# Optimization experiments

Measured on AMD Instinct MI355X. Metric: run time of the kernel, lower is better.

The kernel has to match this reference:

```python
import jax, jax.numpy as jnp
import numpy as np

EMBED = 1024
HEADS = 16
HEAD_DIM = EMBED // HEADS
HIDDEN = 4096
EPS = 1e-5


def setup_inputs() -> dict:
    key = jax.random.key(0)
    ks = jax.random.split(key, 16)
    s_e = 1.0 / np.sqrt(EMBED)
    s_h = 1.0 / np.sqrt(HIDDEN)
    return {
        "x": jax.random.normal(ks[0], (8, 1024, EMBED), dtype=jnp.float32),
        "ln1_g": jnp.ones((EMBED,), jnp.float32),
        "ln1_b": jnp.zeros((EMBED,), jnp.float32),
        "ln2_g": jnp.ones((EMBED,), jnp.float32),
        "ln2_b": jnp.zeros((EMBED,), jnp.float32),
        "wq": jax.random.uniform(ks[1], (EMBED, EMBED), jnp.float32, -s_e, s_e),
        "bq": jax.random.uniform(ks[2], (EMBED,), jnp.float32, -s_e, s_e),
        "wk": jax.random.uniform(ks[3], (EMBED, EMBED), jnp.float32, -s_e, s_e),
        "bk": jax.random.uniform(ks[4], (EMBED,), jnp.float32, -s_e, s_e),
        "wv": jax.random.uniform(ks[5], (EMBED, EMBED), jnp.float32, -s_e, s_e),
        "bv": jax.random.uniform(ks[6], (EMBED,), jnp.float32, -s_e, s_e),
        "wo": jax.random.uniform(ks[7], (EMBED, EMBED), jnp.float32, -s_e, s_e),
        "bo": jax.random.uniform(ks[8], (EMBED,), jnp.float32, -s_e, s_e),
        "w1": jax.random.uniform(ks[9], (EMBED, HIDDEN), jnp.float32, -s_e, s_e),
        "b1": jax.random.uniform(ks[10], (HIDDEN,), jnp.float32, -s_e, s_e),
        "w2": jax.random.uniform(ks[11], (HIDDEN, EMBED), jnp.float32, -s_h, s_h),
        "b2": jax.random.uniform(ks[12], (EMBED,), jnp.float32, -s_h, s_h),
    }


def _layernorm(x, g, b):
    mu = jnp.mean(x, axis=-1, keepdims=True)
    var = jnp.mean((x - mu) ** 2, axis=-1, keepdims=True)
    return (x - mu) * jax.lax.rsqrt(var + EPS) * g + b


def reference(x, ln1_g, ln1_b, ln2_g, ln2_b, wq, bq, wk, bk, wv, bv, wo, bo, w1, b1, w2, b2):
    B, N, E = x.shape
    scale = HEAD_DIM ** (-0.5)
    # --- attention sublayer (pre-norm) ---
    h = _layernorm(x, ln1_g, ln1_b)
    q = (h @ wq + bq).reshape(B, N, HEADS, HEAD_DIM).transpose(0, 2, 1, 3) * scale
    k = (h @ wk + bk).reshape(B, N, HEADS, HEAD_DIM).transpose(0, 2, 1, 3)
    v = (h @ wv + bv).reshape(B, N, HEADS, HEAD_DIM).transpose(0, 2, 1, 3)
    scores = jnp.einsum("bhqd,bhkd->bhqk", q, k)
    attn = jax.nn.softmax(scores, axis=-1)
    ctx = jnp.einsum("bhqk,bhkd->bhqd", attn, v)
    ctx = ctx.transpose(0, 2, 1, 3).reshape(B, N, E)
    x = x + (ctx @ wo + bo)
    # --- FFN sublayer (pre-norm) ---
    h2 = _layernorm(x, ln2_g, ln2_b)
    ff = jax.nn.relu(h2 @ w1 + b1) @ w2 + b2
    return x + ff
```

## Files before the change

kernel.cpp:

```cpp
#include <hip/hip_runtime.h>
#include <hip/hip_bf16.h>

typedef __attribute__((ext_vector_type(4))) float f32x4;
typedef __attribute__((ext_vector_type(8))) __bf16 bf16x8;
typedef __attribute__((ext_vector_type(4))) __bf16 bf16x4;

static constexpr int E    = 1024;
static constexpr int TOK  = 8192;
static constexpr int HID  = 4096;

#define DEVINL __device__ __forceinline__

DEVINL void gload16(const void* g, void* l) {
  __builtin_amdgcn_global_load_lds((__attribute__((address_space(1))) void*)g,
                                   (__attribute__((address_space(3))) void*)l, 16, 0, 0);
}

__global__ __launch_bounds__(256) void wconv_kernel(const float* __restrict__ W,
                                                    __bf16* __restrict__ Wt,
                                                    int K, int N) {
  __shared__ float tile[32][33];
  const int t  = threadIdx.x;
  const long k0 = (long)blockIdx.y * 32;
  const long n0 = (long)blockIdx.x * 32;
  const int r  = t >> 3;
  const int c4 = (t & 7) * 4;
  float4 v = *(const float4*)&W[(k0 + r) * N + n0 + c4];
  tile[r][c4 + 0] = v.x; tile[r][c4 + 1] = v.y;
  tile[r][c4 + 2] = v.z; tile[r][c4 + 3] = v.w;
  __syncthreads();
  bf16x4 o;
#pragma unroll
  for (int i = 0; i < 4; ++i) o[i] = (__bf16)tile[c4 + i][r];
  *(bf16x4*)&Wt[(n0 + r) * K + k0 + c4] = o;
}

__global__ __launch_bounds__(256) void ln_kernel(const float* __restrict__ X,
                                                 const float* __restrict__ g,
                                                 const float* __restrict__ be,
                                                 __bf16* __restrict__ O) {
  const int t = threadIdx.x;
  const long row = blockIdx.x;
  float4 v = *(const float4*)&X[row * E + t * 4];
  float s  = v.x + v.y + v.z + v.w;
  float ss = v.x * v.x + v.y * v.y + v.z * v.z + v.w * v.w;
#pragma unroll
  for (int off = 32; off; off >>= 1) {
    s  += __shfl_down(s, off);
    ss += __shfl_down(ss, off);
  }
  __shared__ float red[8];
  const int w = t >> 6;
  if ((t & 63) == 0) { red[w] = s; red[4 + w] = ss; }
  __syncthreads();
  s  = red[0] + red[1] + red[2] + red[3];
  ss = red[4] + red[5] + red[6] + red[7];
  const float mean = s * (1.0f / E);
  const float var  = ss * (1.0f / E) - mean * mean;
  const float rstd = rsqrtf(var + 1e-5f);
  float4 gv = *(const float4*)&g[t * 4];
  float4 bv = *(const float4*)&be[t * 4];
  bf16x4 o;
  o[0] = (__bf16)((v.x - mean) * rstd * gv.x + bv.x);
  o[1] = (__bf16)((v.y - mean) * rstd * gv.y + bv.y);
  o[2] = (__bf16)((v.z - mean) * rstd * gv.z + bv.z);
  o[3] = (__bf16)((v.w - mean) * rstd * gv.w + bv.w);
  *(bf16x4*)&O[row * E + t * 4] = o;
}

#define ABAR()  asm volatile("s_barrier" ::: "memory")
#define AVM(n)  asm volatile("s_waitcnt vmcnt(" #n ")" ::: "memory")

template <bool RELU, bool RESID, bool OUTBF, int NB>
__global__ __launch_bounds__(512, 2) void gemm8_kernel(const __bf16* __restrict__ A,
                                                       const __bf16* __restrict__ Bt,
                                                       const float* __restrict__ bias0,
                                                       const float* __restrict__ bias1,
                                                       const float* __restrict__ bias2,
                                                       const float* resid,
                                                       void* Cout,
                                                       int M, int N, int K) {
  extern __shared__ char lds[];
  const int tid  = threadIdx.x;
  const int lane = tid & 63;
  const int l15  = lane & 15;
  const int wid  = tid >> 6;
  const int wr   = wid >> 2;
  const int wc   = wid & 3;

  const int nwg  = gridDim.x * gridDim.y;
  const int flat = blockIdx.x + gridDim.x * blockIdx.y;
  const int swz  = (flat & 7) * (nwg >> 3) + (flat >> 3);
  const int bx   = swz % gridDim.x;
  const int by   = swz / gridDim.x;
  const long brow = (long)by * 256;
  const long bcol = (long)bx * 128;

  const __bf16* Ab = A  + brow * K;
  const __bf16* Bb = Bt + bcol * K;
  const int NT = K >> 6;

  char* bA0 = lds;
  char* bA1 = lds + 49152;
  char* bA2 = lds + 98304;

  auto stageA = [&](int k0, char* base, int seg0, int seg1) {
    {
      const int r = seg0 + (tid >> 3);
      const int p = (tid & 7) ^ (r & 7);
      gload16(Ab + (long)r * K + k0 + p * 8, base + seg0 * 128 + tid * 16);
    }
    {
      const int r = seg1 + (tid >> 3);
      const int p = (tid & 7) ^ (r & 7);
      gload16(Ab + (long)r * K + k0 + p * 8, base + seg1 * 128 + tid * 16);
    }
  };
  auto stageB = [&](int k0, char* base) {
#pragma unroll
    for (int i = 0; i < 2; ++i) {
      const int c = i * 64 + (tid >> 3);
      const int p = (tid & 7) ^ (c & 7);
      gload16(Bb + (long)c * K + k0 + p * 8, base + 32768 + i * 8192 + tid * 16);
    }
  };

  f32x4 acc[8][2];
  const f32x4 z4 = {0.f, 0.f, 0.f, 0.f};
#pragma unroll
  for (int m = 0; m < 8; ++m) { acc[m][0] = z4; acc[m][1] = z4; }

  stageA(0, bA0, 0, 128);
  stageA(0, bA0, 64, 192);
  stageB(0, bA0);
  stageA(64, bA1, 0, 128);
  stageA(64, bA1, 64, 192);
  stageB(64, bA1);
  AVM(6);
  ABAR();

  for (int t = 0; t < NT; ++t) {
    const int k2 = (t + 2 < NT) ? ((t + 2) << 6) : 0;

    bf16x8 af[4][2], bfr[2][2];
#pragma unroll
    for (int m = 0; m < 4; ++m)
#pragma unroll
      for (int kk = 0; kk < 2; ++kk) {
        const int row = wr * 128 + m * 16 + l15;
        const int p   = ((kk << 2) + (lane >> 4)) ^ (row & 7);
        af[m][kk] = *(const bf16x8*)(bA0 + row * 128 + p * 16);
      }
#pragma unroll
    for (int n = 0; n < 2; ++n)
#pragma unroll
      for (int kk = 0; kk < 2; ++kk) {
        const int col = wc * 32 + n * 16 + l15;
        const int p   = ((kk << 2) + (lane >> 4)) ^ (col & 7);
        bfr[n][kk] = *(const bf16x8*)(bA0 + 32768 + col * 128 + p * 16);
      }
    stageA(k2, bA2, 0, 128);
    stageB(k2, bA2);
    ABAR();
    __builtin_amdgcn_s_setprio(1);
#pragma unroll
    for (int m = 0; m < 4; ++m)
#pragma unroll
      for (int n = 0; n < 2; ++n) {
        acc[m][n] = __builtin_amdgcn_mfma_f32_16x16x32_bf16(af[m][0], bfr[n][0], acc[m][n], 0, 0, 0);
        acc[m][n] = __builtin_amdgcn_mfma_f32_16x16x32_bf16(af[m][1], bfr[n][1], acc[m][n], 0, 0, 0);
      }
    __builtin_amdgcn_s_setprio(0);
    ABAR();

#pragma unroll
    for (int m = 0; m < 4; ++m)
#pragma unroll
      for (int kk = 0; kk < 2; ++kk) {
        const int row = wr * 128 + (m + 4) * 16 + l15;
        const int p   = ((kk << 2) + (lane >> 4)) ^ (row & 7);
        af[m][kk] = *(const bf16x8*)(bA0 + row * 128 + p * 16);
      }
    stageA(k2, bA2, 64, 192);
    ABAR();
    __builtin_amdgcn_s_setprio(1);
#pragma unroll
    for (int m = 0; m < 4; ++m)
#pragma unroll
      for (int n = 0; n < 2; ++n) {
        acc[m + 4][n] = __builtin_amdgcn_mfma_f32_16x16x32_bf16(af[m][0], bfr[n][0], acc[m + 4][n], 0, 0, 0);
        acc[m + 4][n] = __builtin_amdgcn_mfma_f32_16x16x32_bf16(af[m][1], bfr[n][1], acc[m + 4][n], 0, 0, 0);
      }
    __builtin_amdgcn_s_setprio(0);
    AVM(6);
    ABAR();

    char* tmp = bA0; bA0 = bA1; bA1 = bA2; bA2 = tmp;
  }
  AVM(0);

#pragma unroll
  for (int m = 0; m < 8; ++m) {
#pragma unroll
    for (int n = 0; n < 2; ++n) {
      const long col = bcol + wc * 32 + n * 16 + l15;
      float bb;
      if (NB == 3) {
        const float* bp = (col < 1024) ? bias0 : ((col < 2048) ? bias1 : bias2);
        bb = bp[col & 1023];
      } else {
        bb = bias0[col];
      }
#pragma unroll
      for (int j = 0; j < 4; ++j) {
        const long row = brow + wr * 128 + m * 16 + (lane >> 4) * 4 + j;
        float val = acc[m][n][j] + bb;
        if (RELU) val = fmaxf(val, 0.f);
        const long idx = row * N + col;
        if (RESID) val += resid[idx];
        if (OUTBF) ((__bf16*)Cout)[idx] = (__bf16)val;
        else       ((float*)Cout)[idx]  = val;
      }
    }
  }
}

__global__ __launch_bounds__(256) void attn_kernel(const __bf16* __restrict__ QKV,
                                                   __bf16* __restrict__ Og) {
  __shared__ __align__(16) __bf16 Qs[64 * 64];
  __shared__ __align__(16) __bf16 Ks[64 * 64];
  __shared__ __align__(16) __bf16 Vt[64 * 64];
  __shared__ __align__(16) __bf16 Ps[4 * 16 * 64];

  const int QSTR = 3072;
  const int t    = threadIdx.x;
  const int lane = t & 63;
  const int w    = t >> 6;
  const int b    = blockIdx.y >> 4;
  const int hh   = blockIdx.y & 15;
  const long row0 = (long)b * 1024 + (long)blockIdx.x * 64;
  const int colQ  = hh * 64;
  const int colK  = colQ + 1024;
  const int colV  = colQ + 2048;

#pragma unroll
  for (int j = 0; j < 2; ++j) {
    const int c = j * 256 + t;
    const int r = c >> 3;
    const int p = (c & 7) ^ (r & 7);
    gload16(QKV + (row0 + r) * QSTR + colQ + p * 8, (char*)Qs + c * 16);
  }

  f32x4 ctx[4];
  float m[4], l[4];
  const f32x4 z4 = {0.f, 0.f, 0.f, 0.f};
#pragma unroll
  for (int i = 0; i < 4; ++i) { ctx[i] = z4; m[i] = -INFINITY; l[i] = 0.f; }

  for (int kb = 0; kb < 16; ++kb) {
    __syncthreads();
    const long krow0 = (long)b * 1024 + kb * 64;
#pragma unroll
    for (int j = 0; j < 2; ++j) {
      const int c = j * 256 + t;
      const int r = c >> 3;
      const int p = (c & 7) ^ (r & 7);
      gload16(QKV + (krow0 + r) * QSTR + colK + p * 8, (char*)Ks + c * 16);
    }
#pragma unroll
    for (int j = 0; j < 2; ++j) {
      const int c = j * 256 + t;
      const int key = c >> 3, dc = c & 7;
      bf16x8 vv = *(const bf16x8*)(QKV + (krow0 + key) * QSTR + colV + dc * 8);
#pragma unroll
      for (int e = 0; e < 8; ++e) {
        const int row = dc * 8 + e;
        const int sw  = (row & 7) ^ ((row >> 3) & 7);
        *(__bf16*)((char*)Vt + ((row * 128 + key * 2) ^ (sw << 4))) = vv[e];
      }
    }
    __syncthreads();

    f32x4 s[4];
#pragma unroll
    for (int nf = 0; nf < 4; ++nf) s[nf] = z4;
#pragma unroll
    for (int kk = 0; kk < 2; ++kk) {
      const int qrow = w * 16 + (lane & 15);
      const int qp   = (kk * 4 + (lane >> 4)) ^ (qrow & 7);
      bf16x8 aq = *(const bf16x8*)((const char*)Qs + qrow * 128 + qp * 16);
#pragma unroll
      for (int nf = 0; nf < 4; ++nf) {
        const int krow = nf * 16 + (lane & 15);
        const int kp   = (kk * 4 + (lane >> 4)) ^ (krow & 7);
        bf16x8 bk = *(const bf16x8*)((const char*)Ks + krow * 128 + kp * 16);
        s[nf] = __builtin_amdgcn_mfma_f32_16x16x32_bf16(aq, bk, s[nf], 0, 0, 0);
      }
    }
#pragma unroll
    for (int nf = 0; nf < 4; ++nf)
#pragma unroll
      for (int j = 0; j < 4; ++j) s[nf][j] *= 0.125f;

#pragma unroll
    for (int j = 0; j < 4; ++j) {
      float mx = fmaxf(fmaxf(s[0][j], s[1][j]), fmaxf(s[2][j], s[3][j]));
#pragma unroll
      for (int off = 1; off < 16; off <<= 1) mx = fmaxf(mx, __shfl_xor(mx, off, 16));
      const float mn   = fmaxf(m[j], mx);
      const float corr = __expf(m[j] - mn);
      float rs = 0.f;
      const int prow = (lane >> 4) * 4 + j;
#pragma unroll
      for (int nf = 0; nf < 4; ++nf) {
        const float p = __expf(s[nf][j] - mn);
        rs += p;
        const int col = nf * 16 + (lane & 15);
        *(__bf16*)((char*)Ps + w * 2048 +
                   ((prow * 128 + col * 2) ^ ((prow & 7) << 4))) = (__bf16)p;
      }
#pragma unroll
      for (int off = 1; off < 16; off <<= 1) rs += __shfl_xor(rs, off, 16);
      l[j] = l[j] * corr + rs;
      m[j] = mn;
#pragma unroll
      for (int df = 0; df < 4; ++df) ctx[df][j] *= corr;
    }

#pragma unroll
    for (int kk = 0; kk < 2; ++kk) {
      const int prow = lane & 15;
      const int pp   = (kk * 4 + (lane >> 4)) ^ (prow & 7);
      bf16x8 ap = *(const bf16x8*)((const char*)Ps + w * 2048 + prow * 128 + pp * 16);
#pragma unroll
      for (int df = 0; df < 4; ++df) {
        const int vrow = df * 16 + (lane & 15);
        const int sw   = (vrow & 7) ^ ((vrow >> 3) & 7);
        const int vp   = (kk * 4 + (lane >> 4)) ^ sw;
        bf16x8 bv = *(const bf16x8*)((const char*)Vt + vrow * 128 + vp * 16);
        ctx[df] = __builtin_amdgcn_mfma_f32_16x16x32_bf16(ap, bv, ctx[df], 0, 0, 0);
      }
    }
  }

#pragma unroll
  for (int df = 0; df < 4; ++df)
#pragma unroll
    for (int j = 0; j < 4; ++j) {
      const long row = row0 + w * 16 + (lane >> 4) * 4 + j;
      const int  col = colQ + df * 16 + (lane & 15);
      Og[row * E + col] = (__bf16)(ctx[df][j] / l[j]);
    }
}

extern "C" void kernel_launch(void* const* d_in, const int* in_sizes, int n_in,
                              void* d_out, int out_size, void* d_ws, size_t ws_size,
                              hipStream_t stream) {
  const float* x     = (const float*)d_in[0];
  const float* ln1g  = (const float*)d_in[1];
  const float* ln1b  = (const float*)d_in[2];
  const float* ln2g  = (const float*)d_in[3];
  const float* ln2b  = (const float*)d_in[4];
  const float* wq    = (const float*)d_in[5];
  const float* bq    = (const float*)d_in[6];
  const float* wk    = (const float*)d_in[7];
  const float* bk    = (const float*)d_in[8];
  const float* wv    = (const float*)d_in[9];
  const float* bv    = (const float*)d_in[10];
  const float* wo    = (const float*)d_in[11];
  const float* bo    = (const float*)d_in[12];
  const float* w1    = (const float*)d_in[13];
  const float* b1    = (const float*)d_in[14];
  const float* w2    = (const float*)d_in[15];
  const float* b2    = (const float*)d_in[16];
  float* out = (float*)d_out;

  char* ws = (char*)d_ws;
  const size_t MB = 1024 * 1024;
  __bf16* Wqkv = (__bf16*)(ws + 0 * MB);
  __bf16* Wot  = (__bf16*)(ws + 6 * MB);
  __bf16* W1t  = (__bf16*)(ws + 8 * MB);
  __bf16* W2t  = (__bf16*)(ws + 16 * MB);
  __bf16* h    = (__bf16*)(ws + 24 * MB);
  __bf16* qkv  = (__bf16*)(ws + 40 * MB);
  __bf16* ctx  = (__bf16*)(ws + 88 * MB);
  __bf16* ff1  = (__bf16*)(ws + 40 * MB);

  const dim3 blk(256);
  const dim3 blk512(512);
  const size_t GLDS = 147456;

  wconv_kernel<<<dim3(E / 32, E / 32), blk, 0, stream>>>(wq, Wqkv, E, E);
  wconv_kernel<<<dim3(E / 32, E / 32), blk, 0, stream>>>(wk, Wqkv + 1024 * 1024, E, E);
  wconv_kernel<<<dim3(E / 32, E / 32), blk, 0, stream>>>(wv, Wqkv + 2048 * 1024, E, E);
  wconv_kernel<<<dim3(E / 32, E / 32), blk, 0, stream>>>(wo, Wot, E, E);
  wconv_kernel<<<dim3(HID / 32, E / 32), blk, 0, stream>>>(w1, W1t, E, HID);
  wconv_kernel<<<dim3(E / 32, HID / 32), blk, 0, stream>>>(w2, W2t, HID, E);

  ln_kernel<<<TOK, blk, 0, stream>>>(x, ln1g, ln1b, h);

  gemm8_kernel<false, false, true, 3><<<dim3(3072 / 128, TOK / 256), blk512, GLDS, stream>>>(
      h, Wqkv, bq, bk, bv, nullptr, qkv, TOK, 3072, E);

  attn_kernel<<<dim3(16, 128), blk, 0, stream>>>(qkv, ctx);

  gemm8_kernel<false, true, false, 1><<<dim3(E / 128, TOK / 256), blk512, GLDS, stream>>>(
      ctx, Wot, bo, nullptr, nullptr, x, out, TOK, E, E);

  ln_kernel<<<TOK, blk, 0, stream>>>(out, ln2g, ln2b, h);

  gemm8_kernel<true, false, true, 1><<<dim3(HID / 128, TOK / 256), blk512, GLDS, stream>>>(
      h, W1t, b1, nullptr, nullptr, nullptr, ff1, TOK, HID, E);

  gemm8_kernel<false, true, false, 1><<<dim3(E / 128, TOK / 256), blk512, GLDS, stream>>>(
      ff1, W2t, b2, nullptr, nullptr, out, out, TOK, E, HID);
}
```

Before: 432.9 us.

## Rewrite attention with 32x32 MFMA, double-buffered K/V, register-resident P

The attention kernel now processes 128 queries per block, with 32 per wave, using 32x32x16 MFMAs that compute S^T = K·Q^T. This keeps P in registers via cvt_pk and permlane32 swaps instead of round-tripping through LDS. K/V tiles are double-buffered so the next tile's loads overlap compute, leaving one barrier per iteration. Softmax uses lazy rescaling that only runs when the running max grows by a threshold, and the grid is halved. The cost is more register pressure and added complexity, and the lazy-rescale threshold could in principle affect numerics.

New measurement: 371.3 us. 1.17x faster.

```diff
diff --git a/kernel.cpp b/kernel.cpp
--- a/kernel.cpp
+++ b/kernel.cpp
@@ -2,8 +2,10 @@
 #include <hip/hip_bf16.h>
 
 typedef __attribute__((ext_vector_type(4))) float f32x4;
+typedef __attribute__((ext_vector_type(16))) float f32x16;
 typedef __attribute__((ext_vector_type(8))) __bf16 bf16x8;
 typedef __attribute__((ext_vector_type(4))) __bf16 bf16x4;
+typedef __attribute__((ext_vector_type(4))) unsigned int u32x4;
 
 static constexpr int E    = 1024;
 static constexpr int TOK  = 8192;
@@ -15,6 +17,11 @@
   __builtin_amdgcn_global_load_lds((__attribute__((address_space(1))) void*)g,
                                    (__attribute__((address_space(3))) void*)l, 16, 0, 0);
 }
+
+#define ABAR()  asm volatile("s_barrier" ::: "memory")
+#define AVM(n)  asm volatile("s_waitcnt vmcnt(" #n ")" ::: "memory")
+#define CVTPK(dst, lo, hi) asm("v_cvt_pk_bf16_f32 %0, %1, %2" : "=v"(dst) : "v"(lo), "v"(hi))
+#define PLSWAP(a, b) asm("v_permlane32_swap_b32 %0, %1" : "+v"(a), "+v"(b))
 
 __global__ __launch_bounds__(256) void wconv_kernel(const float* __restrict__ W,
                                                     __bf16* __restrict__ Wt,
@@ -68,9 +75,6 @@
   *(bf16x4*)&O[row * E + t * 4] = o;
 }
 
-#define ABAR()  asm volatile("s_barrier" ::: "memory")
-#define AVM(n)  asm volatile("s_waitcnt vmcnt(" #n ")" ::: "memory")
-
 template <bool RELU, bool RESID, bool OUTBF, int NB>
 __global__ __launch_bounds__(512, 2) void gemm8_kernel(const __bf16* __restrict__ A,
                                                        const __bf16* __restrict__ Bt,
@@ -225,131 +229,195 @@
   }
 }
 
-__global__ __launch_bounds__(256) void attn_kernel(const __bf16* __restrict__ QKV,
-                                                   __bf16* __restrict__ Og) {
-  __shared__ __align__(16) __bf16 Qs[64 * 64];
-  __shared__ __align__(16) __bf16 Ks[64 * 64];
-  __shared__ __align__(16) __bf16 Vt[64 * 64];
-  __shared__ __align__(16) __bf16 Ps[4 * 16 * 64];
+__global__ __launch_bounds__(256, 3) void attn_kernel(const __bf16* __restrict__ QKV,
+                                                      __bf16* __restrict__ Og) {
+  __shared__ __align__(16) __bf16 Qs[128 * 64];
+  __shared__ __align__(16) __bf16 Ks[2][64 * 64];
+  __shared__ __align__(16) __bf16 Vt[2][64 * 64];
 
   const int QSTR = 3072;
   const int t    = threadIdx.x;
   const int lane = t & 63;
   const int w    = t >> 6;
+  const int l31  = lane & 31;
+  const int h    = lane >> 5;
   const int b    = blockIdx.y >> 4;
   const int hh   = blockIdx.y & 15;
-  const long row0 = (long)b * 1024 + (long)blockIdx.x * 64;
-  const int colQ  = hh * 64;
-  const int colK  = colQ + 1024;
-  const int colV  = colQ + 2048;
-
+  const long row0 = (long)b * 1024 + (long)blockIdx.x * 128;
+  const long kvrow0 = (long)b * 1024;
+  const int colQ = hh * 64;
+  const int colK = colQ + 1024;
+  const int colV = colQ + 2048;
+
+#pragma unroll
+  for (int j = 0; j < 4; ++j) {
+    const int c = j * 256 + t;
+    const int r = c >> 3;
+    const int p = (c & 7) ^ (r & 7);
+    gload16(QKV + (row0 + r) * QSTR + colQ + p * 8, (char*)Qs + c * 16);
+  }
 #pragma unroll
   for (int j = 0; j < 2; ++j) {
     const int c = j * 256 + t;
     const int r = c >> 3;
     const int p = (c & 7) ^ (r & 7);
-    gload16(QKV + (row0 + r) * QSTR + colQ + p * 8, (char*)Qs + c * 16);
-  }
-
-  f32x4 ctx[4];
-  float m[4], l[4];
-  const f32x4 z4 = {0.f, 0.f, 0.f, 0.f};
-#pragma unroll
-  for (int i = 0; i < 4; ++i) { ctx[i] = z4; m[i] = -INFINITY; l[i] = 0.f; }
+    gload16(QKV + (kvrow0 + r) * QSTR + colK + p * 8, (char*)Ks[0] + c * 16);
+  }
+  bf16x8 vv[2];
+#pragma unroll
+  for (int j = 0; j < 2; ++j) {
+    const int c = j * 256 + t;
+    const int key = c >> 3, dc = c & 7;
+    vv[j] = *(const bf16x8*)(QKV + (kvrow0 + key) * QSTR + colV + dc * 8);
+  }
+  AVM(0);
+#pragma unroll
+  for (int j = 0; j < 2; ++j) {
+    const int c = j * 256 + t;
+    const int key = c >> 3, dc = c & 7;
+#pragma unroll
+    for (int e = 0; e < 8; ++e) {
+      const int d = dc * 8 + e;
+      *(__bf16*)((char*)Vt[0] + d * 128 + (((key >> 3) ^ dc) * 16) + (key & 7) * 2) = vv[j][e];
+    }
+  }
+  __syncthreads();
+
+  bf16x8 bq[4];
+  {
+    const int qrow = w * 32 + l31;
+#pragma unroll
+    for (int kk = 0; kk < 4; ++kk) {
+      const int p = (kk * 2 + h) ^ (qrow & 7);
+      bq[kk] = *(const bf16x8*)((const char*)Qs + qrow * 128 + p * 16);
+    }
+  }
+
+  f32x16 ctx0, ctx1;
+#pragma unroll
+  for (int r = 0; r < 16; ++r) { ctx0[r] = 0.f; ctx1[r] = 0.f; }
+  float m = -INFINITY, l = 0.f;
 
   for (int kb = 0; kb < 16; ++kb) {
-    __syncthreads();
-    const long krow0 = (long)b * 1024 + kb * 64;
+    const int cur = kb & 1, nxt = cur ^ 1;
+    const int kb1 = (kb + 1 < 16) ? kb + 1 : kb;
+    const long kr1 = kvrow0 + kb1 * 64;
+
+#pragma unroll
+    for (int j = 0; j < 2; ++j) {
+      const int c = j * 256 + t;
+      const int key = c >> 3, dc = c & 7;
+      vv[j] = *(const bf16x8*)(QKV + (kr1 + key) * QSTR + colV + dc * 8);
+    }
 #pragma unroll
     for (int j = 0; j < 2; ++j) {
       const int c = j * 256 + t;
       const int r = c >> 3;
       const int p = (c & 7) ^ (r & 7);
-      gload16(QKV + (krow0 + r) * QSTR + colK + p * 8, (char*)Ks + c * 16);
-    }
+      gload16(QKV + (kr1 + r) * QSTR + colK + p * 8, (char*)Ks[nxt] + c * 16);
+    }
+
+    f32x16 s0, s1;
+#pragma unroll
+    for (int r = 0; r < 16; ++r) { s0[r] = 0.f; s1[r] = 0.f; }
+    __builtin_amdgcn_s_setprio(1);
+#pragma unroll
+    for (int kk = 0; kk < 4; ++kk) {
+      const int pce = kk * 2 + h;
+      const int p0i = pce ^ (l31 & 7);
+      bf16x8 ak0 = *(const bf16x8*)((const char*)Ks[cur] + l31 * 128 + p0i * 16);
+      bf16x8 ak1 = *(const bf16x8*)((const char*)Ks[cur] + (32 + l31) * 128 + p0i * 16);
+      s0 = __builtin_amdgcn_mfma_f32_32x32x16_bf16(ak0, bq[kk], s0, 0, 0, 0);
+      s1 = __builtin_amdgcn_mfma_f32_32x32x16_bf16(ak1, bq[kk], s1, 0, 0, 0);
+    }
+    __builtin_amdgcn_s_setprio(0);
+
+    float mx = s0[0];
+#pragma unroll
+    for (int r = 1; r < 16; ++r) mx = fmaxf(mx, s0[r]);
+#pragma unroll
+    for (int r = 0; r < 16; ++r) mx = fmaxf(mx, s1[r]);
+    mx = fmaxf(mx, __shfl_xor(mx, 32));
+
+    if (!__all(mx - m <= 64.f)) {
+      const float mn = fmaxf(m, mx);
+      const float corr = __expf((m - mn) * 0.125f);
+      l *= corr;
+#pragma unroll
+      for (int r = 0; r < 16; ++r) { ctx0[r] *= corr; ctx1[r] *= corr; }
+      m = mn;
+    }
+    f32x16 p0, p1;
+    float rs = 0.f;
+#pragma unroll
+    for (int r = 0; r < 16; ++r) { p0[r] = __expf((s0[r] - m) * 0.125f); rs += p0[r]; }
+#pragma unroll
+    for (int r = 0; r < 16; ++r) { p1[r] = __expf((s1[r] - m) * 0.125f); rs += p1[r]; }
+    rs += __shfl_xor(rs, 32);
+    l += rs;
+
+    AVM(2);
 #pragma unroll
     for (int j = 0; j < 2; ++j) {
       const int c = j * 256 + t;
       const int key = c >> 3, dc = c & 7;
-      bf16x8 vv = *(const bf16x8*)(QKV + (krow0 + key) * QSTR + colV + dc * 8);
 #pragma unroll
       for (int e = 0; e < 8; ++e) {
-        const int row = dc * 8 + e;
-        const int sw  = (row & 7) ^ ((row >> 3) & 7);
-        *(__bf16*)((char*)Vt + ((row * 128 + key * 2) ^ (sw << 4))) = vv[e];
-      }
-    }
+        const int d = dc * 8 + e;
+        *(__bf16*)((char*)Vt[nxt] + d * 128 + (((key >> 3) ^ dc) * 16) + (key & 7) * 2) = vv[j][e];
+      }
+    }
+
+    bf16x8 paf[4];
+#pragma unroll
+    for (int ks = 0; ks < 4; ++ks) {
+      const int base = (ks & 1) * 8;
+      unsigned a0, a1, b0, b1;
+      if (ks < 2) {
+        CVTPK(a0, p0[base + 0], p0[base + 1]);
+        CVTPK(b0, p0[base + 4], p0[base + 5]);
+        CVTPK(a1, p0[base + 2], p0[base + 3]);
+        CVTPK(b1, p0[base + 6], p0[base + 7]);
+      } else {
+        CVTPK(a0, p1[base + 0], p1[base + 1]);
+        CVTPK(b0, p1[base + 4], p1[base + 5]);
+        CVTPK(a1, p1[base + 2], p1[base + 3]);
+        CVTPK(b1, p1[base + 6], p1[base + 7]);
+      }
+      PLSWAP(a0, b0);
+      PLSWAP(a1, b1);
+      u32x4 wv4; wv4[0] = a0; wv4[1] = a1; wv4[2] = b0; wv4[3] = b1;
+      paf[ks] = __builtin_bit_cast(bf16x8, wv4);
+    }
+
+    __builtin_amdgcn_s_setprio(1);
+#pragma unroll
+    for (int ks = 0; ks < 4; ++ks) {
+      const int pce = ks * 2 + h;
+      bf16x8 av0 = *(const bf16x8*)((const char*)Vt[cur] + l31 * 128 + ((pce ^ (l31 >> 3)) * 16));
+      bf16x8 av1 = *(const bf16x8*)((const char*)Vt[cur] + (32 + l31) * 128 + ((pce ^ (4 + (l31 >> 3))) * 16));
+      ctx0 = __builtin_amdgcn_mfma_f32_32x32x16_bf16(av0, paf[ks], ctx0, 0, 0, 0);
+      ctx1 = __builtin_amdgcn_mfma_f32_32x32x16_bf16(av1, paf[ks], ctx1, 0, 0, 0);
+    }
+    __builtin_amdgcn_s_setprio(0);
+
     __syncthreads();
-
-    f32x4 s[4];
-#pragma unroll
-    for (int nf = 0; nf < 4; ++nf) s[nf] = z4;
-#pragma unroll
-    for (int kk = 0; kk < 2; ++kk) {
-      const int qrow = w * 16 + (lane & 15);
-      const int qp   = (kk * 4 + (lane >> 4)) ^ (qrow & 7);
-      bf16x8 aq = *(const bf16x8*)((const char*)Qs + qrow * 128 + qp * 16);
-#pragma unroll
-      for (int nf = 0; nf < 4; ++nf) {
-        const int krow = nf * 16 + (lane & 15);
-        const int kp   = (kk * 4 + (lane >> 4)) ^ (krow & 7);
-        bf16x8 bk = *(const bf16x8*)((const char*)Ks + krow * 128 + kp * 16);
-        s[nf] = __builtin_amdgcn_mfma_f32_16x16x32_bf16(aq, bk, s[nf], 0, 0, 0);
-      }
-    }
-#pragma unroll
-    for (int nf = 0; nf < 4; ++nf)
-#pragma unroll
-      for (int j = 0; j < 4; ++j) s[nf][j] *= 0.125f;
-
-#pragma unroll
-    for (int j = 0; j < 4; ++j) {
-      float mx = fmaxf(fmaxf(s[0][j], s[1][j]), fmaxf(s[2][j], s[3][j]));
-#pragma unroll
-      for (int off = 1; off < 16; off <<= 1) mx = fmaxf(mx, __shfl_xor(mx, off, 16));
-      const float mn   = fmaxf(m[j], mx);
-      const float corr = __expf(m[j] - mn);
-      float rs = 0.f;
-      const int prow = (lane >> 4) * 4 + j;
-#pragma unroll
-      for (int nf = 0; nf < 4; ++nf) {
-        const float p = __expf(s[nf][j] - mn);
-        rs += p;
-        const int col = nf * 16 + (lane & 15);
-        *(__bf16*)((char*)Ps + w * 2048 +
-                   ((prow * 128 + col * 2) ^ ((prow & 7) << 4))) = (__bf16)p;
-      }
-#pragma unroll
-      for (int off = 1; off < 16; off <<= 1) rs += __shfl_xor(rs, off, 16);
-      l[j] = l[j] * corr + rs;
-      m[j] = mn;
-#pragma unroll
-      for (int df = 0; df < 4; ++df) ctx[df][j] *= corr;
-    }
-
-#pragma unroll
-    for (int kk = 0; kk < 2; ++kk) {
-      const int prow = lane & 15;
-      const int pp   = (kk * 4 + (lane >> 4)) ^ (prow & 7);
-      bf16x8 ap = *(const bf16x8*)((const char*)Ps + w * 2048 + prow * 128 + pp * 16);
-#pragma unroll
-      for (int df = 0; df < 4; ++df) {
-        const int vrow = df * 16 + (lane & 15);
-        const int sw   = (vrow & 7) ^ ((vrow >> 3) & 7);
-        const int vp   = (kk * 4 + (lane >> 4)) ^ sw;
-        bf16x8 bv = *(const bf16x8*)((const char*)Vt + vrow * 128 + vp * 16);
-        ctx[df] = __builtin_amdgcn_mfma_f32_16x16x32_bf16(ap, bv, ctx[df], 0, 0, 0);
-      }
-    }
-  }
-
-#pragma unroll
-  for (int df = 0; df < 4; ++df)
-#pragma unroll
-    for (int j = 0; j < 4; ++j) {
-      const long row = row0 + w * 16 + (lane >> 4) * 4 + j;
-      const int  col = colQ + df * 16 + (lane & 15);
-      Og[row * E + col] = (__bf16)(ctx[df][j] / l[j]);
+  }
+
+  const float inv = 1.0f / l;
+  const long orow = row0 + w * 32 + l31;
+#pragma unroll
+  for (int f = 0; f < 2; ++f)
+#pragma unroll
+    for (int tq = 0; tq < 4; ++tq) {
+      bf16x4 o;
+#pragma unroll
+      for (int e = 0; e < 4; ++e) {
+        const float v = (f ? ctx1[tq * 4 + e] : ctx0[tq * 4 + e]) * inv;
+        o[e] = (__bf16)v;
+      }
+      const int col = colQ + f * 32 + tq * 8 + h * 4;
+      *(bf16x4*)&Og[orow * E + col] = o;
     }
 }
 
@@ -402,7 +470,7 @@
   gemm8_kernel<false, false, true, 3><<<dim3(3072 / 128, TOK / 256), blk512, GLDS, stream>>>(
       h, Wqkv, bq, bk, bv, nullptr, qkv, TOK, 3072, E);
 
-  attn_kernel<<<dim3(16, 128), blk, 0, stream>>>(qkv, ctx);
+  attn_kernel<<<dim3(8, 128), blk, 0, stream>>>(qkv, ctx);
 
   gemm8_kernel<false, true, false, 1><<<dim3(E / 128, TOK / 256), blk512, GLDS, stream>>>(
       ctx, Wot, bo, nullptr, nullptr, x, out, TOK, E, E);
```
